# Kernel optimization log

Measured on AMD Instinct MI355X. Metric: run time of the kernel, lower is better.

The kernel has to match this reference:

```python
import jax, jax.numpy as jnp
import numpy as np

B, S, D, F, E = 8, 2048, 768, 3072, 8


def setup_inputs() -> dict:
    key = jax.random.key(0)
    k1, k2, k3, k4 = jax.random.split(key, 4)
    return {
        "hidden_states": jax.random.normal(k1, (B, S, D), dtype=jnp.float32),
        "router_w": jax.random.normal(k2, (D, E), dtype=jnp.float32) * 0.02,
        "w_in": jax.random.normal(k3, (E, D, F), dtype=jnp.float32) * 0.02,
        "w_out": jax.random.normal(k4, (E, F, D), dtype=jnp.float32) * 0.02,
    }


def reference(hidden_states, router_w, w_in, w_out):
    b, s, d = hidden_states.shape
    x = hidden_states.reshape(-1, d)                    # [T, D] tokens
    router_logits = x @ router_w                        # [T, E]
    router_probs_full = jax.nn.softmax(router_logits, axis=-1)
    expert_index = jnp.argmax(router_probs_full, axis=-1)          # top-1 routing
    onehot = jax.nn.one_hot(expert_index, E, dtype=x.dtype)        # [T, E] router_mask
    top_prob = jnp.max(router_probs_full, axis=-1, keepdims=True)  # [T, 1] router_probs

    # Per-expert FFN (relu MLP); every token is processed by exactly one expert,
    # expert outputs overwrite the token (gather/scatter combine in the original).
    y = jnp.zeros_like(x)
    for e in range(E):  # fixed small expert count; weights structurally distinct
        h = jax.nn.relu(x @ w_in[e]) @ w_out[e]
        y = y + onehot[:, e:e + 1] * h

    out = (top_prob * y).reshape(b, s, d)
    return out, router_logits, expert_index
```

## Files before the change

kernel.cpp:

```cpp
#include <hip/hip_runtime.h>
#include <hip/hip_bf16.h>

constexpr int T  = 16384;
constexpr int Dh = 768;
constexpr int Fh = 3072;
constexpr int Eh = 8;
constexpr int MAXT2 = T / 256 + Eh;

typedef unsigned short ushort_t;
typedef __attribute__((ext_vector_type(8))) short  bf16x8;
typedef __attribute__((ext_vector_type(4))) float  f32x4;

static __device__ __forceinline__ ushort_t f2bf(float f) {
    unsigned u = __builtin_bit_cast(unsigned, f);
    u += 0x7FFFu + ((u >> 16) & 1u);
    return (ushort_t)(u >> 16);
}

__global__ __launch_bounds__(1024) void router_kernel(
    const float* __restrict__ x, const float* __restrict__ rw,
    float* __restrict__ logits_out, float* __restrict__ eidx_out,
    float* __restrict__ topp, int* __restrict__ counts, int* __restrict__ perm) {

    __shared__ float rwT[Eh][Dh];
    __shared__ int   sAmax[16];
    __shared__ int   sBase[Eh];

    int tid = threadIdx.x;
    for (int i = tid; i < Dh * Eh; i += 1024) {
        int d = i >> 3, e = i & 7;
        rwT[e][d] = rw[i];
    }
    __syncthreads();

    int wave = tid >> 6, lane = tid & 63;
    int t = blockIdx.x * 16 + wave;
    const float* xr = x + (size_t)t * Dh;

    double acc[Eh];
#pragma unroll
    for (int e = 0; e < Eh; ++e) acc[e] = 0.0;

#pragma unroll
    for (int j = 0; j < Dh / 256; ++j) {
        int d = lane * 4 + j * 256;
        const float4 xv = *(const float4*)(xr + d);
#pragma unroll
        for (int e = 0; e < Eh; ++e) {
            const float4 w = *(const float4*)&rwT[e][d];
            acc[e] += (double)xv.x * (double)w.x + (double)xv.y * (double)w.y
                    + (double)xv.z * (double)w.z + (double)xv.w * (double)w.w;
        }
    }
#pragma unroll
    for (int off = 32; off > 0; off >>= 1) {
#pragma unroll
        for (int e = 0; e < Eh; ++e) acc[e] += __shfl_xor(acc[e], off, 64);
    }

    int amax = 0;
    if (lane == 0) {
        float l32[Eh];
        float m = -3.4e38f;
#pragma unroll
        for (int e = 0; e < Eh; ++e) l32[e] = (float)acc[e];
#pragma unroll
        for (int e = 0; e < Eh; ++e) {
            if (l32[e] > m) { m = l32[e]; amax = e; }
        }
        float s = 0.f;
#pragma unroll
        for (int e = 0; e < Eh; ++e) s += expf(l32[e] - m);
#pragma unroll
        for (int e = 0; e < Eh; ++e) logits_out[(size_t)t * Eh + e] = l32[e];
        eidx_out[t] = (float)amax;
        topp[t]     = 1.0f / s;
        sAmax[wave] = amax;
    }
    __syncthreads();

    if (tid < Eh) {
        int c = 0;
#pragma unroll
        for (int w = 0; w < 16; ++w) c += (sAmax[w] == tid);
        sBase[tid] = (c > 0) ? atomicAdd(&counts[tid], c) : 0;
    }
    __syncthreads();

    if (lane == 0) {
        int prior = 0;
        for (int w = 0; w < wave; ++w) prior += (sAmax[w] == amax);
        perm[amax * T + sBase[amax] + prior] = t;
    }
}

__global__ void scan_counts(const int* counts, int* offsets,
                            int* tE, int* tGoff, int* tSlot0, int* tRows, int* nT) {
    int lane = threadIdx.x;
    if (lane < Eh) {
        int coff = 0, toff = 0;
        for (int e = 0; e < lane; ++e) {
            int ce = counts[e];
            coff += ce;
            toff += (ce + 255) >> 8;
        }
        int c = counts[lane];
        offsets[lane] = coff;
        int myt = (c + 255) >> 8;
        for (int k = 0; k < myt; ++k) {
            int idx = toff + k;
            tE[idx]     = lane;
            tGoff[idx]  = coff + k * 256;
            tSlot0[idx] = k * 256;
            int rem = c - k * 256;
            tRows[idx]  = rem < 256 ? rem : 256;
        }
        if (lane == Eh - 1) {
            offsets[Eh] = coff + c;
            nT[0] = toff + myt;
        }
    }
}

__global__ void gather_cast_x(const float* __restrict__ x, const int* __restrict__ offsets,
                              const int* __restrict__ perm, ushort_t* __restrict__ Xg) {
    __shared__ int soff[Eh + 1];
    if (threadIdx.x < Eh + 1) soff[threadIdx.x] = offsets[threadIdx.x];
    __syncthreads();
    int q  = blockIdx.x * 256 + threadIdx.x;
    int g  = q / (Dh / 4);
    int cq = (q - g * (Dh / 4)) * 4;
    int e = 0;
#pragma unroll
    for (int i = 1; i < Eh; ++i) e += (g >= soff[i]);
    int tok = perm[e * T + (g - soff[e])];
    const float4 v = *(const float4*)(x + (size_t)tok * Dh + cq);
    ushort4 o;
    o.x = f2bf(v.x); o.y = f2bf(v.y); o.z = f2bf(v.z); o.w = f2bf(v.w);
    *(ushort4*)(Xg + (size_t)g * Dh + cq) = o;
}

__global__ __launch_bounds__(256) void transpose_cvt(
    const float* __restrict__ src, ushort_t* __restrict__ dst, int R, int C) {
    __shared__ ushort_t tile[64][65];
    int tid = threadIdx.x;
    size_t base = (size_t)blockIdx.z * (size_t)R * (size_t)C;
    int c0 = blockIdx.x * 64, r0 = blockIdx.y * 64;
    int rr  = tid >> 4;
    int cc4 = (tid & 15) * 4;
#pragma unroll
    for (int p = 0; p < 4; ++p) {
        int r = rr + p * 16;
        const float4 v = *(const float4*)(src + base + (size_t)(r0 + r) * C + c0 + cc4);
        tile[r][cc4 + 0] = f2bf(v.x);
        tile[r][cc4 + 1] = f2bf(v.y);
        tile[r][cc4 + 2] = f2bf(v.z);
        tile[r][cc4 + 3] = f2bf(v.w);
    }
    __syncthreads();
    int co = tid >> 4;
    int rp = (tid & 15) * 4;
#pragma unroll
    for (int p = 0; p < 4; ++p) {
        int c = co + p * 16;
        ushort4 o = { tile[rp][c], tile[rp + 1][c], tile[rp + 2][c], tile[rp + 3][c] };
        *(ushort4*)(dst + base + (size_t)(c0 + c) * R + r0 + rp) = o;
    }
}

template<int KTOT, int NTOT, int MODE>
__global__ __launch_bounds__(512, 2) void moe_gemm2(
    const ushort_t* __restrict__ Aall, const ushort_t* __restrict__ Ball,
    const int* __restrict__ tE, const int* __restrict__ tGoff,
    const int* __restrict__ tSlot0, const int* __restrict__ tRows,
    const int* __restrict__ nT,
    const int* __restrict__ perm, const float* __restrict__ topp,
    void* __restrict__ Cout)
{
    int xcd = blockIdx.x & 7;
    int pos = blockIdx.x >> 3;
    int ytile = pos / 9;
    int i     = xcd * 9 + (pos - ytile * 9);

    if (i >= nT[0]) return;
    int e     = tE[i];
    int goff  = tGoff[i];
    int slot0 = tSlot0[i];
    int rows  = tRows[i];
    int n0    = ytile * 256;

    const ushort_t* Ap = Aall + (size_t)goff * KTOT;
    const ushort_t* Bp = Ball + (size_t)e * KTOT * NTOT + (size_t)n0 * KTOT;

    __shared__ ushort_t As[4][256 * 32];
    __shared__ ushort_t Bs[4][256 * 32];
    __shared__ int   tokLds[256];
    __shared__ float probLds[256];

    int tid = threadIdx.x, lane = tid & 63, wid_w = tid >> 6;
    int wr = wid_w >> 2, wc = wid_w & 3;
    int gq = lane >> 4, lm = lane & 15;
    int lm3 = lm & 3;

    if (MODE == 1 && tid < 256) {
        int tok = (tid < rows) ? perm[e * T + slot0 + tid] : 0;
        tokLds[tid]  = tok;
        probLds[tid] = (tid < rows) ? topp[tok] : 0.f;
    }

    f32x4 acc[8][4];
    const f32x4 zero = {0.f, 0.f, 0.f, 0.f};
#pragma unroll
    for (int mi = 0; mi < 8; ++mi)
#pragma unroll
        for (int ni = 0; ni < 4; ++ni) acc[mi][ni] = zero;

#define STAGE(SLOT, KT) { \
    _Pragma("unroll") \
    for (int j = 0; j < 2; ++j) { \
        int c_ = tid + j * 512; \
        int rr = c_ >> 2, gg = c_ & 3; \
        int srow_ = rr < rows ? rr : rows - 1; \
        const ushort_t* srcA_ = Ap + (size_t)srow_ * KTOT + (size_t)(KT) * 32 + ((gg ^ (rr & 3)) << 3); \
        __builtin_amdgcn_global_load_lds( \
            (const __attribute__((address_space(1))) unsigned int*)srcA_, \
            (__attribute__((address_space(3))) unsigned int*)&As[SLOT][c_ * 8], 16, 0, 0); \
    } \
    _Pragma("unroll") \
    for (int j = 0; j < 2; ++j) { \
        int c_ = tid + j * 512; \
        int rr = c_ >> 2, gg = c_ & 3; \
        const ushort_t* srcB_ = Bp + (size_t)rr * KTOT + (size_t)(KT) * 32 + ((gg ^ (rr & 3)) << 3); \
        __builtin_amdgcn_global_load_lds( \
            (const __attribute__((address_space(1))) unsigned int*)srcB_, \
            (__attribute__((address_space(3))) unsigned int*)&Bs[SLOT][c_ * 8], 16, 0, 0); \
    } }

    const int nkt = KTOT / 32;

    STAGE(0, 0);
    STAGE(1, 1);
    STAGE(2, 2);
    asm volatile("s_waitcnt vmcnt(8)" ::: "memory");
    __builtin_amdgcn_sched_barrier(0);
    __builtin_amdgcn_s_barrier();

    for (int t = 0; t < nkt; ++t) {
        const int SL = t & 3;
        if (t + 3 < nkt) STAGE((t + 3) & 3, t + 3);

        bf16x8 af[8], bb[4];
#pragma unroll
        for (int ni = 0; ni < 4; ++ni)
            bb[ni] = *(const bf16x8*)&Bs[SL][(wc * 64 + ni * 16 + lm) * 32 + ((gq ^ lm3) << 3)];
#pragma unroll
        for (int mi = 0; mi < 8; ++mi)
            af[mi] = *(const bf16x8*)&As[SL][(wr * 128 + mi * 16 + lm) * 32 + ((gq ^ lm3) << 3)];

        __builtin_amdgcn_s_setprio(1);
#pragma unroll
        for (int mi = 0; mi < 8; ++mi)
#pragma unroll
            for (int ni = 0; ni < 4; ++ni)
                acc[mi][ni] = __builtin_amdgcn_mfma_f32_16x16x32_bf16(
                    af[mi], bb[ni], acc[mi][ni], 0, 0, 0);
        __builtin_amdgcn_s_setprio(0);

        if (t + 1 < nkt) {
            if (t + 3 < nkt) {
                asm volatile("s_waitcnt vmcnt(8)" ::: "memory");
            } else if (t + 2 < nkt) {
                asm volatile("s_waitcnt vmcnt(4)" ::: "memory");
            } else {
                asm volatile("s_waitcnt vmcnt(0)" ::: "memory");
            }
            __builtin_amdgcn_sched_barrier(0);
        }
        __builtin_amdgcn_s_barrier();
    }

    int cr = (lane >> 4) * 4;
    int cc = lane & 15;
#pragma unroll
    for (int mi = 0; mi < 8; ++mi) {
#pragma unroll
        for (int r = 0; r < 4; ++r) {
            int m = wr * 128 + mi * 16 + cr + r;
            if (m < rows) {
                if (MODE == 0) {
                    ushort_t* hp = (ushort_t*)Cout + (size_t)(goff + m) * NTOT
                                 + n0 + wc * 64 + cc;
#pragma unroll
                    for (int ni = 0; ni < 4; ++ni) {
                        float v = acc[mi][ni][r];
                        hp[ni * 16] = f2bf(v > 0.f ? v : 0.f);
                    }
                } else {
                    int tok = tokLds[m];
                    float p = probLds[m];
                    float* op = (float*)Cout + (size_t)tok * NTOT
                              + n0 + wc * 64 + cc;
#pragma unroll
                    for (int ni = 0; ni < 4; ++ni) op[ni * 16] = acc[mi][ni][r] * p;
                }
            }
        }
    }
#undef STAGE
}

constexpr size_t OFF_COUNTS  = 0;
constexpr size_t OFF_OFFSETS = 256;
constexpr size_t OFF_TILES   = 512;
constexpr size_t OFF_TOPP    = OFF_TILES + 4 * 144 * 5 + 64;
constexpr size_t OFF_PERM    = OFF_TOPP + (size_t)T * 4;
constexpr size_t OFF_XG      = (OFF_PERM + (size_t)Eh * T * 4 + 255) & ~(size_t)255;
constexpr size_t OFF_H       = (OFF_XG + (size_t)(T + 128) * Dh * 2 + 255) & ~(size_t)255;
constexpr size_t OFF_WIN     = (OFF_H + (size_t)(T + 128) * Fh * 2 + 255) & ~(size_t)255;
constexpr size_t OFF_WOUT    = (OFF_WIN + (size_t)Eh * Dh * Fh * 2 + 255) & ~(size_t)255;

extern "C" void kernel_launch(void* const* d_in, const int* in_sizes, int n_in,
                              void* d_out, int out_size, void* d_ws, size_t ws_size,
                              hipStream_t stream) {
    const float* x    = (const float*)d_in[0];
    const float* rw   = (const float*)d_in[1];
    const float* w_in = (const float*)d_in[2];
    const float* w_out= (const float*)d_in[3];

    float* out    = (float*)d_out;
    float* logits = out + (size_t)T * Dh;
    float* eidx   = logits + (size_t)T * Eh;

    char* ws = (char*)d_ws;
    int*      counts  = (int*)(ws + OFF_COUNTS);
    int*      offsets = (int*)(ws + OFF_OFFSETS);
    int*      tE      = (int*)(ws + OFF_TILES);
    int*      tGoff   = tE + 144;
    int*      tSlot0  = tGoff + 144;
    int*      tRows   = tSlot0 + 144;
    int*      nT      = tRows + 144;
    float*    topp    = (float*)(ws + OFF_TOPP);
    int*      perm    = (int*)(ws + OFF_PERM);
    ushort_t* Xg      = (ushort_t*)(ws + OFF_XG);
    ushort_t* h       = (ushort_t*)(ws + OFF_H);
    ushort_t* WinT    = (ushort_t*)(ws + OFF_WIN);
    ushort_t* WoutT   = (ushort_t*)(ws + OFF_WOUT);

    hipMemsetAsync(counts, 0, Eh * sizeof(int), stream);
    router_kernel<<<T / 16, 1024, 0, stream>>>(x, rw, logits, eidx, topp, counts, perm);
    scan_counts<<<1, 64, 0, stream>>>(counts, offsets, tE, tGoff, tSlot0, tRows, nT);
    gather_cast_x<<<(T * (Dh / 4)) / 256, 256, 0, stream>>>(x, offsets, perm, Xg);
    transpose_cvt<<<dim3(Fh / 64, Dh / 64, Eh), 256, 0, stream>>>(w_in, WinT, Dh, Fh);
    transpose_cvt<<<dim3(Dh / 64, Fh / 64, Eh), 256, 0, stream>>>(w_out, WoutT, Fh, Dh);
    moe_gemm2<Dh, Fh, 0><<<dim3(MAXT2 * (Fh / 256)), 512, 0, stream>>>(
        Xg, WinT, tE, tGoff, tSlot0, tRows, nT, perm, topp, (void*)h);
    moe_gemm2<Fh, Dh, 1><<<dim3(MAXT2 * (Dh / 256)), 512, 0, stream>>>(
        h, WoutT, tE, tGoff, tSlot0, tRows, nT, perm, topp, (void*)out);
}
```

Before: 532.6 us.

## Shrink MoE GEMM row tiles to 128, use K=64 single-buffered stages, raise occupancy

After: 471.0 us. 11.6% less time.

```diff
diff --git a/kernel.cpp b/kernel.cpp
--- a/kernel.cpp
+++ b/kernel.cpp
@@ -5,7 +5,7 @@
 constexpr int Dh = 768;
 constexpr int Fh = 3072;
 constexpr int Eh = 8;
-constexpr int MAXT2 = T / 256 + Eh;
+constexpr int ROWT = T / 128 + Eh;
 
 typedef unsigned short ushort_t;
 typedef __attribute__((ext_vector_type(8))) short  bf16x8;
@@ -94,30 +94,29 @@
     }
 }
 
-__global__ void scan_counts(const int* counts, int* offsets,
-                            int* tE, int* tGoff, int* tSlot0, int* tRows, int* nT) {
+__global__ void scan_counts(const int* counts, int* offsets, int* L) {
     int lane = threadIdx.x;
     if (lane < Eh) {
         int coff = 0, toff = 0;
         for (int e = 0; e < lane; ++e) {
             int ce = counts[e];
             coff += ce;
-            toff += (ce + 255) >> 8;
+            toff += (ce + 127) >> 7;
         }
         int c = counts[lane];
         offsets[lane] = coff;
-        int myt = (c + 255) >> 8;
+        int myt = (c + 127) >> 7;
         for (int k = 0; k < myt; ++k) {
             int idx = toff + k;
-            tE[idx]     = lane;
-            tGoff[idx]  = coff + k * 256;
-            tSlot0[idx] = k * 256;
-            int rem = c - k * 256;
-            tRows[idx]  = rem < 256 ? rem : 256;
+            L[idx]       = lane;
+            L[160 + idx] = coff + k * 128;
+            L[320 + idx] = k * 128;
+            int rem = c - k * 128;
+            L[480 + idx] = rem < 128 ? rem : 128;
         }
         if (lane == Eh - 1) {
             offsets[Eh] = coff + c;
-            nT[0] = toff + myt;
+            L[640] = toff + myt;
         }
     }
 }
@@ -169,7 +168,7 @@
 }
 
 template<int KTOT, int NTOT, int MODE>
-__global__ __launch_bounds__(512, 2) void moe_gemm2(
+__global__ __launch_bounds__(512, 4) void moe_gemm3(
     const ushort_t* __restrict__ Aall, const ushort_t* __restrict__ Ball,
     const int* __restrict__ tE, const int* __restrict__ tGoff,
     const int* __restrict__ tSlot0, const int* __restrict__ tRows,
@@ -177,10 +176,11 @@
     const int* __restrict__ perm, const float* __restrict__ topp,
     void* __restrict__ Cout)
 {
-    int xcd = blockIdx.x & 7;
-    int pos = blockIdx.x >> 3;
-    int ytile = pos / 9;
-    int i     = xcd * 9 + (pos - ytile * 9);
+    int b   = blockIdx.x;
+    int xcd = b & 7;
+    int pos = b >> 3;
+    int ytile = pos / 17;
+    int i     = xcd * 17 + (pos - ytile * 17);
 
     if (i >= nT[0]) return;
     int e     = tE[i];
@@ -192,100 +192,85 @@
     const ushort_t* Ap = Aall + (size_t)goff * KTOT;
     const ushort_t* Bp = Ball + (size_t)e * KTOT * NTOT + (size_t)n0 * KTOT;
 
-    __shared__ ushort_t As[4][256 * 32];
-    __shared__ ushort_t Bs[4][256 * 32];
-    __shared__ int   tokLds[256];
-    __shared__ float probLds[256];
-
-    int tid = threadIdx.x, lane = tid & 63, wid_w = tid >> 6;
-    int wr = wid_w >> 2, wc = wid_w & 3;
-    int gq = lane >> 4, lm = lane & 15;
-    int lm3 = lm & 3;
-
-    if (MODE == 1 && tid < 256) {
+    __shared__ ushort_t As[128 * 64];
+    __shared__ ushort_t Bs[256 * 64];
+    __shared__ int   tokLds[MODE ? 128 : 1];
+    __shared__ float probLds[MODE ? 128 : 1];
+
+    int tid = threadIdx.x, lane = tid & 63, wid = tid >> 6;
+    int wr = wid >> 2, wc = wid & 3;
+    int gq = lane >> 4, lm = lane & 15, l7 = lane & 7;
+
+    if (MODE == 1 && tid < 128) {
         int tok = (tid < rows) ? perm[e * T + slot0 + tid] : 0;
         tokLds[tid]  = tok;
         probLds[tid] = (tid < rows) ? topp[tok] : 0.f;
     }
 
-    f32x4 acc[8][4];
+    f32x4 acc[4][4];
     const f32x4 zero = {0.f, 0.f, 0.f, 0.f};
 #pragma unroll
-    for (int mi = 0; mi < 8; ++mi)
+    for (int mi = 0; mi < 4; ++mi)
 #pragma unroll
         for (int ni = 0; ni < 4; ++ni) acc[mi][ni] = zero;
 
-#define STAGE(SLOT, KT) { \
-    _Pragma("unroll") \
-    for (int j = 0; j < 2; ++j) { \
-        int c_ = tid + j * 512; \
-        int rr = c_ >> 2, gg = c_ & 3; \
-        int srow_ = rr < rows ? rr : rows - 1; \
-        const ushort_t* srcA_ = Ap + (size_t)srow_ * KTOT + (size_t)(KT) * 32 + ((gg ^ (rr & 3)) << 3); \
-        __builtin_amdgcn_global_load_lds( \
-            (const __attribute__((address_space(1))) unsigned int*)srcA_, \
-            (__attribute__((address_space(3))) unsigned int*)&As[SLOT][c_ * 8], 16, 0, 0); \
-    } \
-    _Pragma("unroll") \
-    for (int j = 0; j < 2; ++j) { \
-        int c_ = tid + j * 512; \
-        int rr = c_ >> 2, gg = c_ & 3; \
-        const ushort_t* srcB_ = Bp + (size_t)rr * KTOT + (size_t)(KT) * 32 + ((gg ^ (rr & 3)) << 3); \
-        __builtin_amdgcn_global_load_lds( \
-            (const __attribute__((address_space(1))) unsigned int*)srcB_, \
-            (__attribute__((address_space(3))) unsigned int*)&Bs[SLOT][c_ * 8], 16, 0, 0); \
-    } }
-
-    const int nkt = KTOT / 32;
-
-    STAGE(0, 0);
-    STAGE(1, 1);
-    STAGE(2, 2);
-    asm volatile("s_waitcnt vmcnt(8)" ::: "memory");
-    __builtin_amdgcn_sched_barrier(0);
-    __builtin_amdgcn_s_barrier();
+    const int nkt = KTOT / 64;
 
     for (int t = 0; t < nkt; ++t) {
-        const int SL = t & 3;
-        if (t + 3 < nkt) STAGE((t + 3) & 3, t + 3);
-
-        bf16x8 af[8], bb[4];
+#pragma unroll
+        for (int j = 0; j < 2; ++j) {
+            int c_ = tid + j * 512;
+            int rr = c_ >> 3, gg = c_ & 7;
+            int srow_ = rr < rows ? rr : rows - 1;
+            const ushort_t* src_ = Ap + (size_t)srow_ * KTOT + t * 64 + ((gg ^ (rr & 7)) << 3);
+            __builtin_amdgcn_global_load_lds(
+                (const __attribute__((address_space(1))) unsigned int*)src_,
+                (__attribute__((address_space(3))) unsigned int*)&As[c_ * 8], 16, 0, 0);
+        }
+#pragma unroll
+        for (int j = 0; j < 4; ++j) {
+            int c_ = tid + j * 512;
+            int rr = c_ >> 3, gg = c_ & 7;
+            const ushort_t* src_ = Bp + (size_t)rr * KTOT + t * 64 + ((gg ^ (rr & 7)) << 3);
+            __builtin_amdgcn_global_load_lds(
+                (const __attribute__((address_space(1))) unsigned int*)src_,
+                (__attribute__((address_space(3))) unsigned int*)&Bs[c_ * 8], 16, 0, 0);
+        }
+        asm volatile("s_waitcnt vmcnt(0)" ::: "memory");
+        __builtin_amdgcn_sched_barrier(0);
+        __builtin_amdgcn_s_barrier();
+
+        bf16x8 bb[4][2];
 #pragma unroll
         for (int ni = 0; ni < 4; ++ni)
-            bb[ni] = *(const bf16x8*)&Bs[SL][(wc * 64 + ni * 16 + lm) * 32 + ((gq ^ lm3) << 3)];
-#pragma unroll
-        for (int mi = 0; mi < 8; ++mi)
-            af[mi] = *(const bf16x8*)&As[SL][(wr * 128 + mi * 16 + lm) * 32 + ((gq ^ lm3) << 3)];
+#pragma unroll
+            for (int ks = 0; ks < 2; ++ks)
+                bb[ni][ks] = *(const bf16x8*)&Bs[
+                    (wc * 64 + ni * 16 + lm) * 64 + ((((ks << 2) + gq) ^ l7) << 3)];
 
         __builtin_amdgcn_s_setprio(1);
 #pragma unroll
-        for (int mi = 0; mi < 8; ++mi)
-#pragma unroll
-            for (int ni = 0; ni < 4; ++ni)
-                acc[mi][ni] = __builtin_amdgcn_mfma_f32_16x16x32_bf16(
-                    af[mi], bb[ni], acc[mi][ni], 0, 0, 0);
+        for (int mi = 0; mi < 4; ++mi) {
+            int arow = (wr * 64 + mi * 16 + lm) * 64;
+            bf16x8 af0 = *(const bf16x8*)&As[arow + ((gq ^ l7) << 3)];
+            bf16x8 af1 = *(const bf16x8*)&As[arow + (((4 + gq) ^ l7) << 3)];
+#pragma unroll
+            for (int ni = 0; ni < 4; ++ni) {
+                acc[mi][ni] = __builtin_amdgcn_mfma_f32_16x16x32_bf16(af0, bb[ni][0], acc[mi][ni], 0, 0, 0);
+                acc[mi][ni] = __builtin_amdgcn_mfma_f32_16x16x32_bf16(af1, bb[ni][1], acc[mi][ni], 0, 0, 0);
+            }
+        }
         __builtin_amdgcn_s_setprio(0);
-
-        if (t + 1 < nkt) {
-            if (t + 3 < nkt) {
-                asm volatile("s_waitcnt vmcnt(8)" ::: "memory");
-            } else if (t + 2 < nkt) {
-                asm volatile("s_waitcnt vmcnt(4)" ::: "memory");
-            } else {
-                asm volatile("s_waitcnt vmcnt(0)" ::: "memory");
-            }
-            __builtin_amdgcn_sched_barrier(0);
-        }
         __builtin_amdgcn_s_barrier();
     }
 
     int cr = (lane >> 4) * 4;
     int cc = lane & 15;
 #pragma unroll
-    for (int mi = 0; mi < 8; ++mi) {
+    for (int mi = 0; mi < 4; ++mi) {
 #pragma unroll
         for (int r = 0; r < 4; ++r) {
-            int m = wr * 128 + mi * 16 + cr + r;
+            int m = wr * 64 + mi * 16 + cr + r;
             if (m < rows) {
                 if (MODE == 0) {
                     ushort_t* hp = (ushort_t*)Cout + (size_t)(goff + m) * NTOT
@@ -306,13 +291,12 @@
             }
         }
     }
-#undef STAGE
 }
 
 constexpr size_t OFF_COUNTS  = 0;
 constexpr size_t OFF_OFFSETS = 256;
 constexpr size_t OFF_TILES   = 512;
-constexpr size_t OFF_TOPP    = OFF_TILES + 4 * 144 * 5 + 64;
+constexpr size_t OFF_TOPP    = OFF_TILES + 3328;
 constexpr size_t OFF_PERM    = OFF_TOPP + (size_t)T * 4;
 constexpr size_t OFF_XG      = (OFF_PERM + (size_t)Eh * T * 4 + 255) & ~(size_t)255;
 constexpr size_t OFF_H       = (OFF_XG + (size_t)(T + 128) * Dh * 2 + 255) & ~(size_t)255;
@@ -334,11 +318,12 @@
     char* ws = (char*)d_ws;
     int*      counts  = (int*)(ws + OFF_COUNTS);
     int*      offsets = (int*)(ws + OFF_OFFSETS);
-    int*      tE      = (int*)(ws + OFF_TILES);
-    int*      tGoff   = tE + 144;
-    int*      tSlot0  = tGoff + 144;
-    int*      tRows   = tSlot0 + 144;
-    int*      nT      = tRows + 144;
+    int*      L       = (int*)(ws + OFF_TILES);
+    int*      tE      = L;
+    int*      tGoff   = L + 160;
+    int*      tSlot0  = L + 320;
+    int*      tRows   = L + 480;
+    int*      nT      = L + 640;
     float*    topp    = (float*)(ws + OFF_TOPP);
     int*      perm    = (int*)(ws + OFF_PERM);
     ushort_t* Xg      = (ushort_t*)(ws + OFF_XG);
@@ -348,12 +333,12 @@
 
     hipMemsetAsync(counts, 0, Eh * sizeof(int), stream);
     router_kernel<<<T / 16, 1024, 0, stream>>>(x, rw, logits, eidx, topp, counts, perm);
-    scan_counts<<<1, 64, 0, stream>>>(counts, offsets, tE, tGoff, tSlot0, tRows, nT);
+    scan_counts<<<1, 64, 0, stream>>>(counts, offsets, L);
     gather_cast_x<<<(T * (Dh / 4)) / 256, 256, 0, stream>>>(x, offsets, perm, Xg);
     transpose_cvt<<<dim3(Fh / 64, Dh / 64, Eh), 256, 0, stream>>>(w_in, WinT, Dh, Fh);
     transpose_cvt<<<dim3(Dh / 64, Fh / 64, Eh), 256, 0, stream>>>(w_out, WoutT, Fh, Dh);
-    moe_gemm2<Dh, Fh, 0><<<dim3(MAXT2 * (Fh / 256)), 512, 0, stream>>>(
+    moe_gemm3<Dh, Fh, 0><<<dim3(ROWT * (Fh / 256)), 512, 0, stream>>>(
         Xg, WinT, tE, tGoff, tSlot0, tRows, nT, perm, topp, (void*)h);
-    moe_gemm2<Fh, Dh, 1><<<dim3(MAXT2 * (Dh / 256)), 512, 0, stream>>>(
+    moe_gemm3<Fh, Dh, 1><<<dim3(ROWT * (Dh / 256)), 512, 0, stream>>>(
         h, WoutT, tE, tGoff, tSlot0, tRows, nT, perm, topp, (void*)out);
 }
```
